# Performance work log

Hardware: AMD Instinct MI355X
Metric: run time of the kernel (lower is better)

## Reference

```python
import jax, jax.numpy as jnp
import numpy as np

B, T, HID = 2, 1024, 1024
NQ, NK, DK, DV = 8, 4, 128, 128
KDIM, KKDIM, KVDIM, VDIM = NQ * DK, NK * DK, NK * DV, NQ * DV  # 1024, 512, 512, 1024
CONV_DIM = KDIM + KKDIM + KVDIM  # 2048
KSZ = 4
EPS = 1e-5


def setup_inputs() -> dict:
    ks = jax.random.split(jax.random.key(0), 6)
    tot = KDIM + KKDIM + KVDIM + VDIM + NQ + NQ  # 3104
    return {
        "x": jax.random.normal(ks[0], (B, T, HID), jnp.float32),
        "w_in": jax.random.normal(ks[1], (HID, tot), jnp.float32) * 0.02,
        "conv_w": jax.random.normal(ks[2], (CONV_DIM, KSZ), jnp.float32) * 0.3,
        "A_log": jax.random.uniform(ks[3], (NQ,), jnp.float32, 0.0, 1.0),
        "dt_bias": jnp.ones((NQ,), jnp.float32),
        "norm_w": jnp.ones((DV,), jnp.float32),
        "w_out": jax.random.normal(ks[4], (VDIM, HID), jnp.float32) * 0.02,
    }


def _l2norm(u):
    return u * jax.lax.rsqrt(jnp.sum(u * u, axis=-1, keepdims=True) + 1e-6)


def _forward(x, w_in, conv_w, A_log, dt_bias, norm_w, w_out):
    # merged input projection -> q | k | v | z(gate) | b(beta) | a(decay)
    mixed = x @ w_in  # [B,T,3104]
    o1, o2, o3, o4, o5 = KDIM, KDIM + KKDIM, KDIM + KKDIM + KVDIM, KDIM + KKDIM + KVDIM + VDIM, KDIM + KKDIM + KVDIM + VDIM + NQ
    q, k, v, z, b, a = jnp.split(mixed, [o1, o2, o3, o4, o5], axis=-1)

    # short causal depthwise conv over concatenated q,k,v + silu
    qkv = jnp.concatenate([q, k, v], axis=-1)  # [B,T,CONV_DIM]
    pad = jnp.pad(qkv, ((0, 0), (KSZ - 1, 0), (0, 0)))
    conv = sum(pad[:, j:j + T, :] * conv_w[:, j] for j in range(KSZ))
    qkv = jax.nn.silu(conv)
    q, k, v = jnp.split(qkv, [KDIM, KDIM + KKDIM], axis=-1)

    q = q.reshape(B, T, NQ, DK)
    k = k.reshape(B, T, NK, DK)
    v = v.reshape(B, T, NK, DV)
    # GQA: repeat kv heads to q heads (kv_proj_rank is None -> plain repeat)
    rep = NQ // NK
    k = jnp.repeat(k, rep, axis=2)
    v = jnp.repeat(v, rep, axis=2)

    # qk l2-norm in kernel + query scaling
    q = _l2norm(q) * (DK ** -0.5)
    k = _l2norm(k)

    beta = jax.nn.sigmoid(b)                                # [B,T,NQ]
    g = -jnp.exp(A_log) * jax.nn.softplus(a + dt_bias)      # [B,T,NQ] log-decay

    tm = lambda u: jnp.moveaxis(u, 1, 0)  # time-major for scan

    def step(S, inp):
        # S: [B,NQ,DK,DV]
        qt, kt, vt, gt, bt = inp
        S = S * jnp.exp(gt)[..., None, None]
        vt = bt[..., None] * (vt - jnp.einsum('bhk,bhkv->bhv', kt, S))
        S = S + kt[..., None] * vt[..., None, :]
        ot = jnp.einsum('bhk,bhkv->bhv', qt, S)
        return S, ot

    S0 = jnp.zeros((B, NQ, DK, DV), x.dtype)
    _, o = jax.lax.scan(step, S0, (tm(q), tm(k), tm(v), tm(g), tm(beta)))
    o = jnp.moveaxis(o, 0, 1)  # [B,T,NQ,DV]

    # gated RMS norm with z, then output projection
    zz = z.reshape(B, T, NQ, DV)
    o = o * jax.lax.rsqrt(jnp.mean(o * o, axis=-1, keepdims=True) + EPS)
    o = o * norm_w * jax.nn.silu(zz)
    return o.reshape(B, T, VDIM) @ w_out


def reference(x, w_in, conv_w, A_log, dt_bias, norm_w, w_out):
    return _forward(x, w_in, conv_w, A_log, dt_bias, norm_w, w_out)
```

## Files before the change

kernel.cpp:

```cpp
#include <hip/hip_runtime.h>
#include <hip/hip_bf16.h>
#include <math.h>

#define BB    2
#define TT    1024
#define HID   1024
#define NQ    8
#define NK    4
#define DK    128
#define DV    128
#define TOT   3088
#define CONVD 2048
#define KSZ   4
#define BT    (BB*TT)
#define CHUNK 64
#define NCHUNK (TT/CHUNK)
#define NBH   (BB*NQ)
#define NPAD1 3200
#define JW    32

typedef __attribute__((ext_vector_type(8))) short short8v;
typedef __attribute__((ext_vector_type(4))) float f32x4;
typedef unsigned short ushort_t;
typedef unsigned int uint_t;

__device__ __forceinline__ float siluf(float x)     { return x / (1.f + expf(-x)); }
__device__ __forceinline__ float sigmoidf_(float x) { return 1.f / (1.f + expf(-x)); }
__device__ __forceinline__ float softplusf_(float x){ return x > 15.f ? x : log1pf(expf(x)); }

__device__ __forceinline__ ushort_t f2bf(float f) {
    uint_t u = __builtin_bit_cast(uint_t, f);
    u = (u + 0x7fff + ((u >> 16) & 1)) >> 16;
    return (ushort_t)u;
}
__device__ __forceinline__ float bf2f(ushort_t u) {
    uint_t v = ((uint_t)u) << 16;
    return __builtin_bit_cast(float, v);
}
__device__ __forceinline__ ushort4 pack4(f32x4 v) {
    ushort4 p; p.x = f2bf(v[0]); p.y = f2bf(v[1]); p.z = f2bf(v[2]); p.w = f2bf(v[3]);
    return p;
}

__device__ __forceinline__ void lds_barrier() {
    asm volatile("s_waitcnt lgkmcnt(0)" ::: "memory");
    __builtin_amdgcn_s_barrier();
}

__device__ __forceinline__ void transpose_body(const float* __restrict__ src,
                                               ushort_t* __restrict__ dst,
                                               int K, int N, int bx, int by) {
    __shared__ float tile[32][33];
    int n0 = bx * 32, k0 = by * 32;
    int c = threadIdx.x & 31, rbase = threadIdx.x >> 5;
    #pragma unroll
    for (int i = 0; i < 4; i++) {
        int r = rbase + i * 8;
        int n = n0 + c;
        tile[r][c] = (n < N) ? src[(size_t)(k0 + r) * N + n] : 0.f;
    }
    __syncthreads();
    #pragma unroll
    for (int i = 0; i < 4; i++) {
        int r = rbase + i * 8;
        dst[(size_t)(n0 + r) * K + k0 + c] = f2bf(tile[c][r]);
    }
}

__global__ __launch_bounds__(256) void prep_kernel(const float* __restrict__ x,
                                                   const float* __restrict__ w_in,
                                                   const float* __restrict__ w_out,
                                                   ushort_t* __restrict__ xb,
                                                   ushort_t* __restrict__ bt1,
                                                   ushort_t* __restrict__ bt2) {
    int bid = blockIdx.x;
    if (bid < 2048) {
        int i = (bid * 256 + threadIdx.x) * 4;
        float4 v = *(const float4*)(x + i);
        ushort4 o;
        o.x = f2bf(v.x); o.y = f2bf(v.y); o.z = f2bf(v.z); o.w = f2bf(v.w);
        *(ushort4*)(xb + i) = o;
    } else if (bid < 2048 + 3200) {
        int t = bid - 2048;
        transpose_body(w_in, bt1, HID, TOT, t % 100, t / 100);
    } else {
        int t = bid - 5248;
        transpose_body(w_out, bt2, HID, HID, t % 32, t / 32);
    }
}

__global__ __launch_bounds__(256) void gemm_bf16(const ushort_t* __restrict__ A,
                                                 const ushort_t* __restrict__ BTm,
                                                 float* __restrict__ C,
                                                 int K, int Nc, int ldc) {
    __shared__ ushort_t As[128 * 32];
    __shared__ ushort_t Bs[128 * 32];
    int tid = threadIdx.x;
    int wave = tid >> 6, lane = tid & 63;
    int wr = wave >> 1, wc = wave & 1;
    int row0 = blockIdx.y * 128, col0 = blockIdx.x * 128;

    f32x4 zero4 = {0.f, 0.f, 0.f, 0.f};
    f32x4 acc[4][4];
    #pragma unroll
    for (int m = 0; m < 4; m++)
        #pragma unroll
        for (int n = 0; n < 4; n++) acc[m][n] = zero4;

    int srow = wave * 32 + (lane >> 2);
    int koff = (lane & 3) * 8;
    const ushort_t* gA0 = A + (size_t)(row0 + srow) * K + koff;
    const ushort_t* gA1 = A + (size_t)(row0 + srow + 16) * K + koff;
    const ushort_t* gB0 = BTm + (size_t)(col0 + srow) * K + koff;
    const ushort_t* gB1 = BTm + (size_t)(col0 + srow + 16) * K + koff;
    ushort_t* lA0 = As + (wave * 2 + 0) * 512;
    ushort_t* lA1 = As + (wave * 2 + 1) * 512;
    ushort_t* lB0 = Bs + (wave * 2 + 0) * 512;
    ushort_t* lB1 = Bs + (wave * 2 + 1) * 512;

    for (int k0 = 0; k0 < K; k0 += 32) {
        __builtin_amdgcn_global_load_lds(
            (const __attribute__((address_space(1))) void*)(gA0 + k0),
            (__attribute__((address_space(3))) void*)lA0, 16, 0, 0);
        __builtin_amdgcn_global_load_lds(
            (const __attribute__((address_space(1))) void*)(gA1 + k0),
            (__attribute__((address_space(3))) void*)lA1, 16, 0, 0);
        __builtin_amdgcn_global_load_lds(
            (const __attribute__((address_space(1))) void*)(gB0 + k0),
            (__attribute__((address_space(3))) void*)lB0, 16, 0, 0);
        __builtin_amdgcn_global_load_lds(
            (const __attribute__((address_space(1))) void*)(gB1 + k0),
            (__attribute__((address_space(3))) void*)lB1, 16, 0, 0);
        __syncthreads();

        short8v af[4], bf[4];
        #pragma unroll
        for (int m = 0; m < 4; m++)
            af[m] = *(const short8v*)(As + (wr * 64 + m * 16 + (lane & 15)) * 32 + (lane >> 4) * 8);
        #pragma unroll
        for (int n = 0; n < 4; n++)
            bf[n] = *(const short8v*)(Bs + (wc * 64 + n * 16 + (lane & 15)) * 32 + (lane >> 4) * 8);
        #pragma unroll
        for (int m = 0; m < 4; m++)
            #pragma unroll
            for (int n = 0; n < 4; n++)
                acc[m][n] = __builtin_amdgcn_mfma_f32_16x16x32_bf16(af[m], bf[n], acc[m][n], 0, 0, 0);
        __syncthreads();
    }

    #pragma unroll
    for (int m = 0; m < 4; m++) {
        #pragma unroll
        for (int n = 0; n < 4; n++) {
            int row = row0 + wr * 64 + m * 16 + (lane >> 4) * 4;
            int col = col0 + wc * 64 + n * 16 + (lane & 15);
            if (col < Nc) {
                #pragma unroll
                for (int e = 0; e < 4; e++)
                    C[(size_t)(row + e) * ldc + col] = acc[m][n][e];
            }
        }
    }
}

__global__ __launch_bounds__(256) void conv_split_kernel(const float* __restrict__ mixed,
                                                         const float* __restrict__ conv_w,
                                                         const float* __restrict__ A_log,
                                                         const float* __restrict__ dt_bias,
                                                         ushort_t* __restrict__ qb,
                                                         ushort_t* __restrict__ kb,
                                                         float* __restrict__ kn,
                                                         float* __restrict__ vn,
                                                         float* __restrict__ beta,
                                                         float* __restrict__ g) {
    int raw = blockIdx.x;
    int bt = ((raw & 7) << 8) | (raw >> 3);
    int t = bt & (TT - 1);
    int tid = threadIdx.x;
    int c0 = tid * 8;

    float val[8];
    #pragma unroll
    for (int i = 0; i < 8; i++) val[i] = 0.f;
    #pragma unroll
    for (int j = 0; j < KSZ; j++) {
        int tt = t - (KSZ - 1) + j;
        if (tt >= 0) {
            const float* src = mixed + (size_t)(bt - (KSZ - 1) + j) * TOT + c0;
            #pragma unroll
            for (int i = 0; i < 8; i++) val[i] += src[i] * conv_w[(c0 + i) * KSZ + j];
        }
    }
    #pragma unroll
    for (int i = 0; i < 8; i++) val[i] = siluf(val[i]);

    float ss = 0.f;
    #pragma unroll
    for (int i = 0; i < 8; i++) ss += val[i] * val[i];
    #pragma unroll
    for (int m = 1; m < 16; m <<= 1) ss += __shfl_xor(ss, m, 64);
    float rs = rsqrtf(ss + 1e-6f);

    if (tid < 128) {
        float sc = rs * 0.08838834764831845f;
        short8v pk;
        #pragma unroll
        for (int i = 0; i < 8; i++) pk[i] = (short)f2bf(val[i] * sc);
        *(short8v*)(qb + (size_t)bt * 1024 + c0) = pk;
    } else if (tid < 192) {
        int o = c0 - 1024;
        short8v pk;
        #pragma unroll
        for (int i = 0; i < 8; i++) {
            float kv = val[i] * rs;
            kn[(size_t)bt * 512 + o + i] = kv;
            pk[i] = (short)f2bf(kv);
        }
        *(short8v*)(kb + (size_t)bt * 512 + o) = pk;
    } else {
        #pragma unroll
        for (int i = 0; i < 8; i++) vn[(size_t)bt * 512 + (c0 - 1536) + i] = val[i];
    }
    if (tid < 8) {
        beta[bt * 8 + tid] = sigmoidf_(mixed[(size_t)bt * TOT + 3072 + tid]);
    } else if (tid < 16) {
        int h = tid - 8;
        g[bt * 8 + h] = -expf(A_log[h]) * softplusf_(mixed[(size_t)bt * TOT + 3080 + h] + dt_bias[h]);
    }
}

__global__ __launch_bounds__(256) void phaseA_kernel(const float* __restrict__ kn,
                                                     const float* __restrict__ vn,
                                                     const float* __restrict__ beta,
                                                     const float* __restrict__ g,
                                                     float* __restrict__ W,
                                                     ushort_t* __restrict__ Znegb,
                                                     ushort_t* __restrict__ knT,
                                                     float* __restrict__ Bvec) {
    int bh = blockIdx.x & 15, c = blockIdx.x >> 4;
    int chunk = bh * 16 + c;
    int b = bh >> 3, h = bh & 7, hk = h >> 1;
    int bt0 = b * TT + c * CHUNK;
    int tid = threadIdx.x;
    int wave = tid >> 6, lane = tid & 63;
    int lr = lane & 15, lg = lane >> 4;

    __shared__ __align__(16) ushort_t kcb[64 * 128];
    __shared__ float Ms[64][65];
    __shared__ float Bv[64], Bev[64], bev[64];

    if (tid < 64) {
        float v = g[(size_t)(bt0 + tid) * 8 + h];
        #pragma unroll
        for (int off = 1; off < 64; off <<= 1) {
            float n = __shfl_up(v, off, 64);
            if (tid >= off) v += n;
        }
        Bv[tid] = v;
        Bev[tid] = expf(v);
        bev[tid] = beta[(size_t)(bt0 + tid) * 8 + h];
        Bvec[chunk * 64 + tid] = v;
    }
    for (int i = tid; i < 1024; i += 256) {
        int r = i >> 4, k16 = i & 15;
        const float* src = kn + (size_t)(bt0 + r) * 512 + hk * 128 + k16 * 8;
        float4 v0 = *(const float4*)src;
        float4 v1 = *(const float4*)(src + 4);
        short8v pk;
        pk[0] = (short)f2bf(v0.x); pk[1] = (short)f2bf(v0.y);
        pk[2] = (short)f2bf(v0.z); pk[3] = (short)f2bf(v0.w);
        pk[4] = (short)f2bf(v1.x); pk[5] = (short)f2bf(v1.y);
        pk[6] = (short)f2bf(v1.z); pk[7] = (short)f2bf(v1.w);
        int a = (r * 256 + k16 * 16) ^ ((r & 7) << 4);
        *(short8v*)((char*)kcb + a) = pk;
    }
    __syncthreads();

    {
        int t_lane = wave * 16 + lr;
        short8v af[4];
        #pragma unroll
        for (int ks = 0; ks < 4; ks++) {
            int a = (t_lane * 256 + ks * 64 + lg * 16) ^ ((t_lane & 7) << 4);
            af[ks] = *(const short8v*)((const char*)kcb + a);
        }
        for (int sb = 0; sb <= wave; sb++) {
            f32x4 macc = {0.f, 0.f, 0.f, 0.f};
            int s_lane = sb * 16 + lr;
            #pragma unroll
            for (int ks = 0; ks < 4; ks++) {
                int a = (s_lane * 256 + ks * 64 + lg * 16) ^ ((s_lane & 7) << 4);
                short8v bfr = *(const short8v*)((const char*)kcb + a);
                macc = __builtin_amdgcn_mfma_f32_16x16x32_bf16(af[ks], bfr, macc, 0, 0, 0);
            }
            #pragma unroll
            for (int e = 0; e < 4; e++) {
                int trow = wave * 16 + lg * 4 + e;
                int scol = sb * 16 + lr;
                Ms[trow][scol] = (scol < trow) ? macc[e] * bev[trow] * expf(Bv[trow] - Bv[scol]) : 0.f;
            }
        }
    }

    float Xr[64];
    if (tid < 128) {
        #pragma unroll
        for (int t = 0; t < 64; t++)
            Xr[t] = bev[t] * vn[(size_t)(bt0 + t) * 512 + hk * 128 + tid];
    } else {
        int r = tid - 128;
        #pragma unroll
        for (int t = 0; t < 64; t++)
            Xr[t] = bev[t] * Bev[t] * kn[(size_t)(bt0 + t) * 512 + hk * 128 + r];
    }
    __syncthreads();

    #pragma unroll
    for (int t = 1; t < 64; t++) {
        float a0 = 0.f, a1 = 0.f, a2 = 0.f, a3 = 0.f;
        #pragma unroll
        for (int s = 0; s + 4 <= t; s += 4) {
            a0 += Ms[t][s] * Xr[s];     a1 += Ms[t][s + 1] * Xr[s + 1];
            a2 += Ms[t][s + 2] * Xr[s + 2]; a3 += Ms[t][s + 3] * Xr[s + 3];
        }
        #pragma unroll
        for (int s = t & ~3; s < t; s++) a0 += Ms[t][s] * Xr[s];
        Xr[t] -= (a0 + a1) + (a2 + a3);
    }

    if (tid < 128) {
        float* Wc = W + (size_t)chunk * 8192 + tid;
        #pragma unroll
        for (int t = 0; t < 64; t++) Wc[t * 128] = Xr[t];
    } else {
        ushort_t* Zc = Znegb + (size_t)chunk * 8192 + (tid - 128);
        #pragma unroll
        for (int t = 0; t < 64; t++) Zc[t * 128] = f2bf(-Xr[t]);
    }

    {
        ushort_t* kT = knT + (size_t)bh * 131072 + c * 64;
        for (int i = tid; i < 8192; i += 256) {
            int r = i >> 6, tt = i & 63;
            int a = (tt * 256 + r * 2) ^ ((tt & 7) << 4);
            kT[(size_t)r * 1024 + tt] = *(const ushort_t*)((const char*)kcb + a);
        }
    }
}

__device__ __forceinline__ int swzSt(int j, int k) {
    int a = j * 256 + k * 2;
    return a ^ ((j & 7) << 4);
}
__device__ __forceinline__ int swzUt(int j, int s) {
    int a = j * 128 + s * 2;
    return a ^ ((j & 7) << 4);
}

__global__ __launch_bounds__(256) void phaseB_mfma(const ushort_t* __restrict__ knT,
                                                   const ushort_t* __restrict__ Znegb,
                                                   const float* __restrict__ W,
                                                   const float* __restrict__ Bvec,
                                                   ushort_t* __restrict__ SallT,
                                                   ushort_t* __restrict__ UTg) {
    int bh = blockIdx.x & 15, cg = blockIdx.x >> 4;
    int j0 = cg * JW;
    int tid = threadIdx.x;
    int wave = tid >> 6, lane = tid & 63;
    int lr = lane & 15, lg = lane >> 4;
    int t0 = wave * 16;

    __shared__ __align__(16) ushort_t St[JW * 128];
    __shared__ __align__(16) ushort_t Ut[JW * 64];

    for (int i = tid * 8; i < JW * 128; i += 2048)
        *(int4*)(St + i) = make_int4(0, 0, 0, 0);

    f32x4 Sacc[2][2];
    #pragma unroll
    for (int fr = 0; fr < 2; fr++)
        #pragma unroll
        for (int fc = 0; fc < 2; fc++) Sacc[fr][fc] = (f32x4){0.f, 0.f, 0.f, 0.f};

    const ushort_t* kTbase = knT + (size_t)bh * 131072;
    int chunk0 = bh * 16;

    short8v za[4], ka[4];
    f32x4 wv[2];
    f32x4 bvv[4];
    float b63;
    {
        const ushort_t* Zc = Znegb + (size_t)chunk0 * 8192;
        #pragma unroll
        for (int ks = 0; ks < 4; ks++)
            za[ks] = *(const short8v*)(Zc + (size_t)(t0 + lr) * 128 + ks * 32 + lg * 8);
        const float* Wc = W + (size_t)chunk0 * 8192 + j0;
        #pragma unroll
        for (int fc = 0; fc < 2; fc++)
            #pragma unroll
            for (int e = 0; e < 4; e++)
                wv[fc][e] = Wc[(size_t)(t0 + lg * 4 + e) * 128 + fc * 16 + lr];
        #pragma unroll
        for (int fr = 0; fr < 2; fr++)
            #pragma unroll
            for (int ss = 0; ss < 2; ss++)
                ka[fr * 2 + ss] = *(const short8v*)(kTbase +
                    (size_t)(wave * 32 + fr * 16 + lr) * 1024 + ss * 32 + lg * 8);
        #pragma unroll
        for (int q = 0; q < 4; q++)
            bvv[q] = *(const f32x4*)(Bvec + chunk0 * 64 + (q >> 1) * 32 + lg * 8 + (q & 1) * 4);
        b63 = Bvec[chunk0 * 64 + 63];
    }

    for (int c = 0; c < NCHUNK; c++) {
        int chunk = chunk0 + c;
        ushort_t* SgT = SallT + (size_t)chunk * 16384;
        #pragma unroll
        for (int fr = 0; fr < 2; fr++)
            #pragma unroll
            for (int fc = 0; fc < 2; fc++) {
                int r0 = wave * 32 + fr * 16 + lg * 4;
                int j = j0 + fc * 16 + lr;
                *(ushort4*)(SgT + (size_t)j * 128 + r0) = pack4(Sacc[fr][fc]);
            }
        f32x4 Uacc[2];
        Uacc[0] = wv[0];
        Uacc[1] = wv[1];

        lds_barrier();

        #pragma unroll
        for (int ks = 0; ks < 4; ks++)
            #pragma unroll
            for (int fc = 0; fc < 2; fc++) {
                short8v sb = *(const short8v*)((const char*)St + swzSt(fc * 16 + lr, ks * 32 + lg * 8));
                Uacc[fc] = __builtin_amdgcn_mfma_f32_16x16x32_bf16(za[ks], sb, Uacc[fc], 0, 0, 0);
            }
        ushort_t* UTc = UTg + (size_t)chunk * 8192;
        #pragma unroll
        for (int fc = 0; fc < 2; fc++) {
            int jl = fc * 16 + lr;
            ushort4 pu = pack4(Uacc[fc]);
            *(ushort4*)(UTc + (size_t)(j0 + jl) * 64 + t0 + lg * 4) = pu;
            *(ushort4*)((char*)Ut + swzUt(jl, t0 + lg * 4)) = pu;
        }
        if (c + 1 < NCHUNK) {
            const ushort_t* Zn = Znegb + (size_t)(chunk + 1) * 8192;
            #pragma unroll
            for (int ks = 0; ks < 4; ks++)
                za[ks] = *(const short8v*)(Zn + (size_t)(t0 + lr) * 128 + ks * 32 + lg * 8);
            const float* Wn = W + (size_t)(chunk + 1) * 8192 + j0;
            #pragma unroll
            for (int fc = 0; fc < 2; fc++)
                #pragma unroll
                for (int e = 0; e < 4; e++)
                    wv[fc][e] = Wn[(size_t)(t0 + lg * 4 + e) * 128 + fc * 16 + lr];
        }
        float gC = expf(b63);
        #pragma unroll
        for (int fr = 0; fr < 2; fr++)
            #pragma unroll
            for (int fc = 0; fc < 2; fc++)
                #pragma unroll
                for (int e = 0; e < 4; e++) Sacc[fr][fc][e] *= gC;

        lds_barrier();

        float eb[2][8];
        #pragma unroll
        for (int ss = 0; ss < 2; ss++)
            #pragma unroll
            for (int e = 0; e < 8; e++)
                eb[ss][e] = expf(b63 - bvv[ss * 2 + (e >> 2)][e & 3]);

        #pragma unroll
        for (int fr = 0; fr < 2; fr++) {
            #pragma unroll
            for (int ss = 0; ss < 2; ss++) {
                short8v a;
                #pragma unroll
                for (int e = 0; e < 8; e++)
                    a[e] = (short)f2bf(bf2f((ushort_t)ka[fr * 2 + ss][e]) * eb[ss][e]);
                #pragma unroll
                for (int fc = 0; fc < 2; fc++) {
                    short8v ub = *(const short8v*)((const char*)Ut + swzUt(fc * 16 + lr, ss * 32 + lg * 8));
                    Sacc[fr][fc] = __builtin_amdgcn_mfma_f32_16x16x32_bf16(a, ub, Sacc[fr][fc], 0, 0, 0);
                }
            }
        }
        if (c + 1 < NCHUNK) {
            #pragma unroll
            for (int fr = 0; fr < 2; fr++)
                #pragma unroll
                for (int ss = 0; ss < 2; ss++)
                    ka[fr * 2 + ss] = *(const short8v*)(kTbase +
                        (size_t)(wave * 32 + fr * 16 + lr) * 1024 + (c + 1) * 64 + ss * 32 + lg * 8);
            #pragma unroll
            for (int q = 0; q < 4; q++)
                bvv[q] = *(const f32x4*)(Bvec + (chunk + 1) * 64 + (q >> 1) * 32 + lg * 8 + (q & 1) * 4);
            b63 = Bvec[(chunk + 1) * 64 + 63];
        }
        #pragma unroll
        for (int fr = 0; fr < 2; fr++)
            #pragma unroll
            for (int fc = 0; fc < 2; fc++) {
                int r = wave * 32 + fr * 16 + lg * 4;
                int j = fc * 16 + lr;
                *(ushort4*)((char*)St + swzSt(j, r)) = pack4(Sacc[fr][fc]);
            }
    }
}

__global__ __launch_bounds__(256) void phaseC_mfma(const ushort_t* __restrict__ qb,
                                                   const ushort_t* __restrict__ kb,
                                                   const ushort_t* __restrict__ UTg,
                                                   const ushort_t* __restrict__ SallT,
                                                   const float* __restrict__ Bvec,
                                                   const float* __restrict__ mixed,
                                                   const float* __restrict__ norm_w,
                                                   ushort_t* __restrict__ ginb) {
    int bh = blockIdx.x & 15, c = blockIdx.x >> 4;
    int chunk = bh * 16 + c;
    int b = bh >> 3, h = bh & 7, hk = h >> 1;
    int bt0 = b * TT + c * CHUNK;
    int tid = threadIdx.x, wave = tid >> 6, lane = tid & 63;
    int lr = lane & 15, lg = lane >> 4;

    __shared__ float Bv[64], Bev[64];
    __shared__ __align__(16) ushort_t Pb[64 * 64];

    if (tid < 64) { float v = Bvec[chunk * 64 + tid]; Bv[tid] = v; Bev[tid] = expf(v); }
    __syncthreads();

    int t_lane = wave * 16 + lr;
    const ushort_t* qrow = qb + (size_t)(bt0 + t_lane) * 1024 + h * 128;
    short8v qa[4];
    #pragma unroll
    for (int ks = 0; ks < 4; ks++) qa[ks] = *(const short8v*)(qrow + ks * 32 + lg * 8);

    #pragma unroll
    for (int sb = 0; sb < 4; sb++) {
        f32x4 pacc = {0.f, 0.f, 0.f, 0.f};
        const ushort_t* krow = kb + (size_t)(bt0 + sb * 16 + lr) * 512 + hk * 128;
        #pragma unroll
        for (int ks = 0; ks < 4; ks++) {
            short8v kf = *(const short8v*)(krow + ks * 32 + lg * 8);
            pacc = __builtin_amdgcn_mfma_f32_16x16x32_bf16(qa[ks], kf, pacc, 0, 0, 0);
        }
        int scol = sb * 16 + lr;
        #pragma unroll
        for (int e = 0; e < 4; e++) {
            int trow = wave * 16 + lg * 4 + e;
            float val = (scol <= trow) ? pacc[e] * expf(Bv[trow] - Bv[scol]) : 0.f;
            int a = (trow * 128 + scol * 2) ^ ((trow & 7) << 4);
            *(ushort_t*)((char*)Pb + a) = f2bf(val);
        }
    }

    float Ge[4];
    #pragma unroll
    for (int e = 0; e < 4; e++) Ge[e] = Bev[wave * 16 + lg * 4 + e];
    const ushort_t* ST = SallT + (size_t)chunk * 16384;
    f32x4 acc[8];
    #pragma unroll
    for (int n = 0; n < 8; n++) {
        acc[n] = (f32x4){0.f, 0.f, 0.f, 0.f};
        int j = n * 16 + lr;
        #pragma unroll
        for (int rs = 0; rs < 4; rs++) {
            short8v sf = *(const short8v*)(ST + (size_t)j * 128 + rs * 32 + lg * 8);
            acc[n] = __builtin_amdgcn_mfma_f32_16x16x32_bf16(qa[rs], sf, acc[n], 0, 0, 0);
        }
        #pragma unroll
        for (int e = 0; e < 4; e++) acc[n][e] *= Ge[e];
    }
    __syncthreads();

    short8v pa[2];
    #pragma unroll
    for (int ks = 0; ks < 2; ks++) {
        int a = (t_lane * 128 + (ks * 32 + lg * 8) * 2) ^ ((t_lane & 7) << 4);
        pa[ks] = *(const short8v*)((const char*)Pb + a);
    }
    const ushort_t* UTc = UTg + (size_t)chunk * 8192;
    #pragma unroll
    for (int n = 0; n < 8; n++) {
        int j = n * 16 + lr;
        #pragma unroll
        for (int ks = 0; ks < 2; ks++) {
            short8v uf = *(const short8v*)(UTc + (size_t)j * 64 + ks * 32 + lg * 8);
            acc[n] = __builtin_amdgcn_mfma_f32_16x16x32_bf16(pa[ks], uf, acc[n], 0, 0, 0);
        }
    }

    float rr[4];
    #pragma unroll
    for (int e = 0; e < 4; e++) {
        float s = 0.f;
        #pragma unroll
        for (int n = 0; n < 8; n++) s += acc[n][e] * acc[n][e];
        #pragma unroll
        for (int m = 1; m < 16; m <<= 1) s += __shfl_xor(s, m, 64);
        rr[e] = rsqrtf(s * (1.f / 128.f) + 1e-5f);
    }
    #pragma unroll
    for (int n = 0; n < 8; n++) {
        int j = n * 16 + lr;
        float nw = norm_w[j];
        #pragma unroll
        for (int e = 0; e < 4; e++) {
            int t = wave * 16 + lg * 4 + e;
            float z = mixed[(size_t)(bt0 + t) * TOT + 2048 + h * 128 + j];
            ginb[(size_t)(bt0 + t) * 1024 + h * 128 + j] =
                f2bf(acc[n][e] * rr[e] * nw * siluf(z));
        }
    }
}

extern "C" void kernel_launch(void* const* d_in, const int* in_sizes, int n_in,
                              void* d_out, int out_size, void* d_ws, size_t ws_size,
                              hipStream_t stream) {
    const float* x       = (const float*)d_in[0];
    const float* w_in    = (const float*)d_in[1];
    const float* conv_w  = (const float*)d_in[2];
    const float* A_log   = (const float*)d_in[3];
    const float* dt_bias = (const float*)d_in[4];
    const float* norm_w  = (const float*)d_in[5];
    const float* w_out   = (const float*)d_in[6];
    float* out = (float*)d_out;

    float* ws = (float*)d_ws;
    float* mixed = ws;
    float* kn    = mixed + (size_t)BT * TOT;
    float* vn    = kn + (size_t)BT * 512;
    float* beta  = vn + (size_t)BT * 512;
    float* gdec  = beta + BT * 8;
    float* Wu    = gdec + BT * 8;
    float* Bvec  = Wu + (size_t)BT * 1024;
    float* qbf   = Bvec + NBH * NCHUNK * 64;
    float* kbf   = qbf + 1048576;
    float* knTf  = kbf + 524288;
    float* Znf   = knTf + 1048576;
    float* UTf   = Znf + 1048576;
    float* SallTf= UTf + 1048576;
    float* bt2f  = SallTf + 2097152;

    ushort_t* qb    = (ushort_t*)qbf;
    ushort_t* kb    = (ushort_t*)kbf;
    ushort_t* knTb  = (ushort_t*)knTf;
    ushort_t* Znegb = (ushort_t*)Znf;
    ushort_t* UTb   = (ushort_t*)UTf;
    ushort_t* SallT = (ushort_t*)SallTf;
    ushort_t* bt2   = (ushort_t*)bt2f;
    ushort_t* xb    = (ushort_t*)SallTf;
    ushort_t* bt1   = (ushort_t*)knTf;
    ushort_t* ginb  = (ushort_t*)qbf;

    prep_kernel<<<6272, 256, 0, stream>>>(x, w_in, w_out, xb, bt1, bt2);

    gemm_bf16<<<dim3(NPAD1 / 128, BT / 128), 256, 0, stream>>>(xb, bt1, mixed, HID, TOT, TOT);

    conv_split_kernel<<<BT, 256, 0, stream>>>(mixed, conv_w, A_log, dt_bias, qb, kb, kn, vn, beta, gdec);

    phaseA_kernel<<<NBH * NCHUNK, 256, 0, stream>>>(kn, vn, beta, gdec, Wu, Znegb, knTb, Bvec);
    phaseB_mfma<<<NBH * 4, 256, 0, stream>>>(knTb, Znegb, Wu, Bvec, SallT, UTb);
    phaseC_mfma<<<NBH * NCHUNK, 256, 0, stream>>>(qb, kb, UTb, SallT, Bvec, mixed, norm_w, ginb);

    gemm_bf16<<<dim3(HID / 128, BT / 128), 256, 0, stream>>>(ginb, bt2, out, HID, HID, HID);
}
```

Measured before the change: 176.7 us.

## Deepen GEMM K-tile to 64 with XOR-swizzled LDS and XCD block remap

```diff
diff --git a/kernel.cpp b/kernel.cpp
--- a/kernel.cpp
+++ b/kernel.cpp
@@ -92,59 +92,62 @@
 __global__ __launch_bounds__(256) void gemm_bf16(const ushort_t* __restrict__ A,
                                                  const ushort_t* __restrict__ BTm,
                                                  float* __restrict__ C,
-                                                 int K, int Nc, int ldc) {
-    __shared__ ushort_t As[128 * 32];
-    __shared__ ushort_t Bs[128 * 32];
+                                                 int K, int Nc, int ldc, int nx) {
+    __shared__ __align__(16) ushort_t As[128 * 64];
+    __shared__ __align__(16) ushort_t Bs[128 * 64];
     int tid = threadIdx.x;
     int wave = tid >> 6, lane = tid & 63;
     int wr = wave >> 1, wc = wave & 1;
-    int row0 = blockIdx.y * 128, col0 = blockIdx.x * 128;
-
-    f32x4 zero4 = {0.f, 0.f, 0.f, 0.f};
+    int lr = lane & 15, lg = lane >> 4;
+
+    int flat = blockIdx.x;
+    int swz = (flat & 7) * ((int)gridDim.x >> 3) + (flat >> 3);
+    int col0 = (swz % nx) * 128, row0 = (swz / nx) * 128;
+
     f32x4 acc[4][4];
     #pragma unroll
     for (int m = 0; m < 4; m++)
         #pragma unroll
-        for (int n = 0; n < 4; n++) acc[m][n] = zero4;
-
-    int srow = wave * 32 + (lane >> 2);
-    int koff = (lane & 3) * 8;
-    const ushort_t* gA0 = A + (size_t)(row0 + srow) * K + koff;
-    const ushort_t* gA1 = A + (size_t)(row0 + srow + 16) * K + koff;
-    const ushort_t* gB0 = BTm + (size_t)(col0 + srow) * K + koff;
-    const ushort_t* gB1 = BTm + (size_t)(col0 + srow + 16) * K + koff;
-    ushort_t* lA0 = As + (wave * 2 + 0) * 512;
-    ushort_t* lA1 = As + (wave * 2 + 1) * 512;
-    ushort_t* lB0 = Bs + (wave * 2 + 0) * 512;
-    ushort_t* lB1 = Bs + (wave * 2 + 1) * 512;
-
-    for (int k0 = 0; k0 < K; k0 += 32) {
-        __builtin_amdgcn_global_load_lds(
-            (const __attribute__((address_space(1))) void*)(gA0 + k0),
-            (__attribute__((address_space(3))) void*)lA0, 16, 0, 0);
-        __builtin_amdgcn_global_load_lds(
-            (const __attribute__((address_space(1))) void*)(gA1 + k0),
-            (__attribute__((address_space(3))) void*)lA1, 16, 0, 0);
-        __builtin_amdgcn_global_load_lds(
-            (const __attribute__((address_space(1))) void*)(gB0 + k0),
-            (__attribute__((address_space(3))) void*)lB0, 16, 0, 0);
-        __builtin_amdgcn_global_load_lds(
-            (const __attribute__((address_space(1))) void*)(gB1 + k0),
-            (__attribute__((address_space(3))) void*)lB1, 16, 0, 0);
+        for (int n = 0; n < 4; n++) acc[m][n] = (f32x4){0.f, 0.f, 0.f, 0.f};
+
+    int srowA = (lane >> 3);
+    int skoff = ((lane & 7) ^ (lane >> 3)) * 8;
+
+    for (int k0 = 0; k0 < K; k0 += 64) {
+        #pragma unroll
+        for (int j = 0; j < 4; j++) {
+            int i = wave * 4 + j;
+            int r = 8 * i + srowA;
+            __builtin_amdgcn_global_load_lds(
+                (const __attribute__((address_space(1))) void*)(A + (size_t)(row0 + r) * K + k0 + skoff),
+                (__attribute__((address_space(3))) void*)(As + i * 512), 16, 0, 0);
+            __builtin_amdgcn_global_load_lds(
+                (const __attribute__((address_space(1))) void*)(BTm + (size_t)(col0 + r) * K + k0 + skoff),
+                (__attribute__((address_space(3))) void*)(Bs + i * 512), 16, 0, 0);
+        }
         __syncthreads();
 
-        short8v af[4], bf[4];
-        #pragma unroll
-        for (int m = 0; m < 4; m++)
-            af[m] = *(const short8v*)(As + (wr * 64 + m * 16 + (lane & 15)) * 32 + (lane >> 4) * 8);
-        #pragma unroll
-        for (int n = 0; n < 4; n++)
-            bf[n] = *(const short8v*)(Bs + (wc * 64 + n * 16 + (lane & 15)) * 32 + (lane >> 4) * 8);
-        #pragma unroll
-        for (int m = 0; m < 4; m++)
-            #pragma unroll
-            for (int n = 0; n < 4; n++)
-                acc[m][n] = __builtin_amdgcn_mfma_f32_16x16x32_bf16(af[m], bf[n], acc[m][n], 0, 0, 0);
+        #pragma unroll
+        for (int kk = 0; kk < 2; kk++) {
+            short8v af[4], bf[4];
+            #pragma unroll
+            for (int m = 0; m < 4; m++) {
+                int row = wr * 64 + m * 16 + lr;
+                int pb = (row * 128 + kk * 64 + lg * 16) ^ ((row & 7) << 4);
+                af[m] = *(const short8v*)((const char*)As + pb);
+            }
+            #pragma unroll
+            for (int n = 0; n < 4; n++) {
+                int row = wc * 64 + n * 16 + lr;
+                int pb = (row * 128 + kk * 64 + lg * 16) ^ ((row & 7) << 4);
+                bf[n] = *(const short8v*)((const char*)Bs + pb);
+            }
+            #pragma unroll
+            for (int m = 0; m < 4; m++)
+                #pragma unroll
+                for (int n = 0; n < 4; n++)
+                    acc[m][n] = __builtin_amdgcn_mfma_f32_16x16x32_bf16(af[m], bf[n], acc[m][n], 0, 0, 0);
+        }
         __syncthreads();
     }
 
@@ -152,8 +155,8 @@
     for (int m = 0; m < 4; m++) {
         #pragma unroll
         for (int n = 0; n < 4; n++) {
-            int row = row0 + wr * 64 + m * 16 + (lane >> 4) * 4;
-            int col = col0 + wc * 64 + n * 16 + (lane & 15);
+            int row = row0 + wr * 64 + m * 16 + lg * 4;
+            int col = col0 + wc * 64 + n * 16 + lr;
             if (col < Nc) {
                 #pragma unroll
                 for (int e = 0; e < 4; e++)
@@ -658,7 +661,7 @@
 
     prep_kernel<<<6272, 256, 0, stream>>>(x, w_in, w_out, xb, bt1, bt2);
 
-    gemm_bf16<<<dim3(NPAD1 / 128, BT / 128), 256, 0, stream>>>(xb, bt1, mixed, HID, TOT, TOT);
+    gemm_bf16<<<400, 256, 0, stream>>>(xb, bt1, mixed, HID, TOT, TOT, NPAD1 / 128);
 
     conv_split_kernel<<<BT, 256, 0, stream>>>(mixed, conv_w, A_log, dt_bias, qb, kb, kn, vn, beta, gdec);
 
@@ -666,5 +669,5 @@
     phaseB_mfma<<<NBH * 4, 256, 0, stream>>>(knTb, Znegb, Wu, Bvec, SallT, UTb);
     phaseC_mfma<<<NBH * NCHUNK, 256, 0, stream>>>(qb, kb, UTb, SallT, Bvec, mixed, norm_w, ginb);
 
-    gemm_bf16<<<dim3(HID / 128, BT / 128), 256, 0, stream>>>(ginb, bt2, out, HID, HID, HID);
-}
+    gemm_bf16<<<128, 256, 0, stream>>>(ginb, bt2, out, HID, HID, HID, HID / 128);
+}
```

Result: faster. 166.6 us (-5.7%).
